# Kernel tuning notes

Hardware: AMD Instinct MI355X
Metric: run time of the kernel (lower is better)

Reference implementation:

```python
import jax, jax.numpy as jnp
import numpy as np

DIM = 1024
NUM_HEADS = 16
HEAD_DIM = DIM // NUM_HEADS
B, S, E = 4, 8192, 2000


def setup_inputs() -> dict:
    key = jax.random.key(0)
    ks = jax.random.split(key, 16)
    sd = 0.02
    inp = {
        "x": jax.random.normal(ks[0], (B, S, DIM), dtype=jnp.float32),
        "src_indices": jax.random.randint(ks[1], (E,), 0, S),
        "dst_indices": jax.random.randint(ks[2], (E,), 0, S),
        # linear weights stored [in, out] (applied as x @ W + b)
        "Wq": jax.random.normal(ks[3], (DIM, DIM), jnp.float32) * sd,
        "bq": jnp.zeros((DIM,), jnp.float32),
        "Wk": jax.random.normal(ks[4], (DIM, DIM), jnp.float32) * sd,
        "bk": jnp.zeros((DIM,), jnp.float32),
        "Wv": jax.random.normal(ks[5], (DIM, DIM), jnp.float32) * sd,
        "bv": jnp.zeros((DIM,), jnp.float32),
        "Wo": jax.random.normal(ks[6], (DIM, DIM), jnp.float32) * sd,
        "bo": jnp.zeros((DIM,), jnp.float32),
        "edge_weight": jax.random.normal(ks[7], (1, NUM_HEADS, 1), jnp.float32),
        "W1": jax.random.normal(ks[8], (2 * HEAD_DIM, HEAD_DIM), jnp.float32) * sd,
        "b1": jnp.zeros((HEAD_DIM,), jnp.float32),
        "W2": jax.random.normal(ks[9], (HEAD_DIM, 1), jnp.float32) * sd,
        "b2": jnp.zeros((1,), jnp.float32),
    }
    return inp


def reference(x, src_indices, dst_indices, Wq, bq, Wk, bk, Wv, bv, Wo, bo,
              edge_weight, W1, b1, W2, b2):
    Bs, Sl, D = x.shape
    H, hd = NUM_HEADS, HEAD_DIM
    scale = hd ** -0.5

    def heads(t):  # [B,S,D] -> [B,H,S,hd]
        return t.reshape(Bs, Sl, H, hd).transpose(0, 2, 1, 3)

    q = heads(x @ Wq + bq)
    k = heads(x @ Wk + bk)
    v = heads(x @ Wv + bv)

    q_src = jnp.take(q, src_indices, axis=2)   # [B,H,E,hd]
    k_dst = jnp.take(k, dst_indices, axis=2)   # [B,H,E,hd]
    v_dst = jnp.take(v, dst_indices, axis=2)   # [B,H,E,hd]

    ef = jnp.concatenate([q_src, k_dst], axis=-1)          # [B,H,E,2hd]
    h = jax.nn.gelu(ef @ W1 + b1, approximate=False)       # [B,H,E,hd]
    scores = (h @ W2 + b2) * scale                         # [B,H,E,1]
    attn = jax.nn.softmax(scores, axis=2)                  # softmax over all edges
    attn = attn * edge_weight[..., None]                   # [1,H,1,1] broadcast

    weighted = attn * v_dst                                # [B,H,E,hd]
    out = jnp.zeros((Bs, H, Sl, hd), x.dtype).at[:, :, src_indices, :].add(weighted)

    final = out.transpose(0, 2, 1, 3).reshape(Bs, Sl, D)
    return final @ Wo + bo
```

## Files before the change

### kernel.cpp

```cpp
#include <hip/hip_runtime.h>
#include <hip/hip_bf16.h>
#include <math.h>

#define DIMK 1024
#define NH 16
#define HD 64
#define BB 4
#define SS 8192
#define EPAD 136

typedef __attribute__((ext_vector_type(8))) short bf16x8;
typedef __attribute__((ext_vector_type(8))) unsigned short ushort8;
typedef __attribute__((ext_vector_type(4))) float f32x4;

#define MFMA16(a, b, c) __builtin_amdgcn_mfma_f32_16x16x32_bf16((a), (b), (c), 0, 0, 0)

__device__ __forceinline__ unsigned short f32_to_bf16_rne(float f) {
  unsigned int u = __float_as_uint(f);
  u = (u + 0x7fffu + ((u >> 16) & 1u)) >> 16;
  return (unsigned short)u;
}
__device__ __forceinline__ float bf16_bits_to_f32(unsigned short b) {
  return __uint_as_float(((unsigned int)b) << 16);
}

__global__ __launch_bounds__(256) void fill_out_kernel(const float4* __restrict__ bo4,
                                                       float4* __restrict__ out, int total4) {
  for (int i = blockIdx.x * 256 + threadIdx.x; i < total4; i += gridDim.x * 256)
    out[i] = bo4[i & 255];
}

__global__ __launch_bounds__(256) void prep_w(const float* __restrict__ W,
                                              unsigned short* __restrict__ WT_hi,
                                              unsigned short* __restrict__ WT_lo) {
  __shared__ float st[64][65];
  const int bk = blockIdx.x * 64, bn = blockIdx.y * 64;
  const int t = threadIdx.x;
  const int lr = t >> 4, lc = (t & 15) * 4;
#pragma unroll
  for (int i = 0; i < 4; i++) {
    int k = lr + i * 16;
    float4 v = *(const float4*)(W + (size_t)(bk + k) * DIMK + bn + lc);
    st[k][lc] = v.x; st[k][lc + 1] = v.y; st[k][lc + 2] = v.z; st[k][lc + 3] = v.w;
  }
  __syncthreads();
#pragma unroll
  for (int i = 0; i < 4; i++) {
    int n = lr + i * 16;
    unsigned long long ph = 0, pl = 0;
#pragma unroll
    for (int j = 0; j < 4; j++) {
      float v = st[lc + j][n];
      unsigned short hb = f32_to_bf16_rne(v);
      unsigned short lb = f32_to_bf16_rne(v - bf16_bits_to_f32(hb));
      ph |= ((unsigned long long)hb) << (16 * j);
      pl |= ((unsigned long long)lb) << (16 * j);
    }
    *(unsigned long long*)(WT_hi + (size_t)(bn + n) * DIMK + bk + lc) = ph;
    *(unsigned long long*)(WT_lo + (size_t)(bn + n) * DIMK + bk + lc) = pl;
  }
}

__global__ __launch_bounds__(256) void prep_w1(const float* __restrict__ W1,
                                               unsigned short* __restrict__ W1Th,
                                               unsigned short* __restrict__ W1Tl) {
  for (int idx = threadIdx.x; idx < 128 * 64; idx += 256) {
    int k = idx >> 6, n = idx & 63;
    float v = W1[idx];
    unsigned short hb = f32_to_bf16_rne(v);
    unsigned short lb = f32_to_bf16_rne(v - bf16_bits_to_f32(hb));
    W1Th[n * 128 + k] = hb;
    W1Tl[n * 128 + k] = lb;
  }
}

__global__ __launch_bounds__(256) void prep_a(const float* __restrict__ X,
                                              const int* __restrict__ gidx,
                                              unsigned short* __restrict__ Ah,
                                              unsigned short* __restrict__ Al, int E) {
  const int row = blockIdx.x;
  const float* sr;
  if (gidx) {
    int b = row / E, e = row - b * E;
    sr = X + ((size_t)b * SS + gidx[e]) * DIMK;
  } else {
    sr = X + (size_t)row * DIMK;
  }
  const int d = threadIdx.x * 4;
  float4 v = *(const float4*)(sr + d);
  float vv[4] = {v.x, v.y, v.z, v.w};
  unsigned long long ph = 0, pl = 0;
#pragma unroll
  for (int i = 0; i < 4; i++) {
    unsigned short hb = f32_to_bf16_rne(vv[i]);
    unsigned short lb = f32_to_bf16_rne(vv[i] - bf16_bits_to_f32(hb));
    ph |= ((unsigned long long)hb) << (16 * i);
    pl |= ((unsigned long long)lb) << (16 * i);
  }
  *(unsigned long long*)(Ah + (size_t)row * DIMK + d) = ph;
  *(unsigned long long*)(Al + (size_t)row * DIMK + d) = pl;
}

__global__ __launch_bounds__(256) void init_table(int* __restrict__ t) {
  t[blockIdx.x * 256 + threadIdx.x] = 0x7fffffff;
}
__global__ __launch_bounds__(256) void build_first(const int* __restrict__ src,
                                                   int* __restrict__ t, int E) {
  int e = blockIdx.x * 256 + threadIdx.x;
  if (e < E) atomicMin(&t[src[e]], e);
}
__global__ __launch_bounds__(256) void read_first(const int* __restrict__ src,
                                                  const int* __restrict__ t,
                                                  int* __restrict__ f, int E) {
  int e = blockIdx.x * 256 + threadIdx.x;
  if (e < E) f[e] = t[src[e]];
}

template <int MODE>
__global__ __launch_bounds__(256) void gemm_bf16p(
    const unsigned short* __restrict__ Ah, const unsigned short* __restrict__ Al,
    const unsigned short* __restrict__ BTh, const unsigned short* __restrict__ BTl,
    const float* __restrict__ bias, const float* __restrict__ bias2,
    float* __restrict__ out, int ldc, int gy,
    const int* __restrict__ fidx, const int* __restrict__ srci, int M, int E) {
  __shared__ unsigned short As_hi[128][40];
  __shared__ unsigned short As_lo[128][40];
  __shared__ unsigned short Bs_hi[128][40];
  __shared__ unsigned short Bs_lo[128][40];

  const int tid = threadIdx.x;
  const int nwg = gridDim.x;
  int w;
  if ((nwg & 7) == 0)
    w = (blockIdx.x & 7) * (nwg >> 3) + (blockIdx.x >> 3);
  else
    w = blockIdx.x;
  const int mt = w / gy, nt = w - mt * gy;
  const int m0 = mt * 128, n0 = nt * 128;

  const int lane = tid & 63, wv = tid >> 6;
  const int wm0 = (wv >> 1) * 64, wn0 = (wv & 1) * 64;

  const int r0 = tid >> 2, q0 = (tid & 3) * 8;
  const int r1 = r0 + 64;
  const size_t a0 = (size_t)((m0 + r0 < M) ? m0 + r0 : M - 1) * DIMK + q0;
  const size_t a1 = (size_t)((m0 + r1 < M) ? m0 + r1 : M - 1) * DIMK + q0;
  const unsigned short* pAh0 = Ah + a0;
  const unsigned short* pAh1 = Ah + a1;
  const unsigned short* pAl0 = Al + a0;
  const unsigned short* pAl1 = Al + a1;
  const size_t b0 = (size_t)(n0 + r0) * DIMK + q0;
  const size_t b1 = (size_t)(n0 + r1) * DIMK + q0;
  const unsigned short* pBh0 = BTh + b0;
  const unsigned short* pBh1 = BTh + b1;
  const unsigned short* pBl0 = BTl + b0;
  const unsigned short* pBl1 = BTl + b1;

  f32x4 acc[4][4];
#pragma unroll
  for (int i = 0; i < 4; i++)
#pragma unroll
    for (int j = 0; j < 4; j++) acc[i][j] = (f32x4){0.f, 0.f, 0.f, 0.f};

  for (int k0 = 0; k0 < DIMK; k0 += 32) {
    ushort8 vAh0 = *(const ushort8*)(pAh0 + k0);
    ushort8 vAh1 = *(const ushort8*)(pAh1 + k0);
    ushort8 vAl0 = *(const ushort8*)(pAl0 + k0);
    ushort8 vAl1 = *(const ushort8*)(pAl1 + k0);
    ushort8 vBh0 = *(const ushort8*)(pBh0 + k0);
    ushort8 vBh1 = *(const ushort8*)(pBh1 + k0);
    ushort8 vBl0 = *(const ushort8*)(pBl0 + k0);
    ushort8 vBl1 = *(const ushort8*)(pBl1 + k0);

    __syncthreads();
    *(ushort8*)&As_hi[r0][q0] = vAh0;
    *(ushort8*)&As_hi[r1][q0] = vAh1;
    *(ushort8*)&As_lo[r0][q0] = vAl0;
    *(ushort8*)&As_lo[r1][q0] = vAl1;
    *(ushort8*)&Bs_hi[r0][q0] = vBh0;
    *(ushort8*)&Bs_hi[r1][q0] = vBh1;
    *(ushort8*)&Bs_lo[r0][q0] = vBl0;
    *(ushort8*)&Bs_lo[r1][q0] = vBl1;
    __syncthreads();

    bf16x8 fah[4], fal[4], fbh[4], fbl[4];
    const int kk = (lane >> 4) * 8;
    const int rr = lane & 15;
#pragma unroll
    for (int f = 0; f < 4; f++) {
      fah[f] = *(bf16x8*)&As_hi[wm0 + f * 16 + rr][kk];
      fal[f] = *(bf16x8*)&As_lo[wm0 + f * 16 + rr][kk];
      fbh[f] = *(bf16x8*)&Bs_hi[wn0 + f * 16 + rr][kk];
      fbl[f] = *(bf16x8*)&Bs_lo[wn0 + f * 16 + rr][kk];
    }
#pragma unroll
    for (int mf = 0; mf < 4; mf++)
#pragma unroll
      for (int nf = 0; nf < 4; nf++) {
        acc[mf][nf] = MFMA16(fah[mf], fbh[nf], acc[mf][nf]);
        acc[mf][nf] = MFMA16(fah[mf], fbl[nf], acc[mf][nf]);
        acc[mf][nf] = MFMA16(fal[mf], fbh[nf], acc[mf][nf]);
      }
  }

  const int cq = lane >> 4, cr = lane & 15;
#pragma unroll
  for (int nf = 0; nf < 4; nf++) {
    const int col = n0 + wn0 + nf * 16 + cr;
    const float bv = (MODE == 0 && bias2 != nullptr && col >= DIMK) ? bias2[col - DIMK]
                                                                    : bias[col & (DIMK - 1)];
#pragma unroll
    for (int mf = 0; mf < 4; mf++) {
#pragma unroll
      for (int r = 0; r < 4; r++) {
        const int mrow = m0 + wm0 + mf * 16 + cq * 4 + r;
        if (mrow >= M) continue;
        if (MODE == 0) {
          out[(size_t)mrow * ldc + col] = acc[mf][nf][r] + bv;
        } else {
          int b = mrow / E, e = mrow - b * E;
          if (fidx[e] == e) {
            int orow = b * SS + srci[e];
            out[(size_t)orow * ldc + col] = acc[mf][nf][r] + bv;
          }
        }
      }
    }
  }
}

__global__ __launch_bounds__(256) void edge_scores_mfma(
    const float* __restrict__ qs, const float* __restrict__ kd, int ldk,
    const unsigned short* __restrict__ W1Th, const unsigned short* __restrict__ W1Tl,
    const float* __restrict__ b1, const float* __restrict__ W2,
    const float* __restrict__ b2, float* __restrict__ scores, int E, int CH) {
  __shared__ unsigned short W1h[64][EPAD], W1l[64][EPAD];
  __shared__ unsigned short EFh[4][16][EPAD], EFl[4][16][EPAD];
  const int tid = threadIdx.x, lane = tid & 63, w = tid >> 6;
  const int bh = blockIdx.x / CH, ch = blockIdx.x - bh * CH;
  const int b = bh >> 4, h = bh & 15;

  for (int idx = tid; idx < 64 * 16; idx += 256) {
    int n = idx >> 4, g = (idx & 15) * 8;
    *(ushort8*)&W1h[n][g] = *(const ushort8*)(W1Th + n * 128 + g);
    *(ushort8*)&W1l[n][g] = *(const ushort8*)(W1Tl + n * 128 + g);
  }
  __syncthreads();

  const int etile = ch * 4 + w;
  const int e0 = etile * 16;
  if (e0 >= E) return;

  const int r = lane >> 2, c0 = (lane & 3) * 16;
  {
    const int er = (e0 + r < E) ? e0 + r : E - 1;
    const float* qrow = qs + ((size_t)(b * E + er)) * DIMK + h * HD + c0;
    const float* krow = kd + ((size_t)(b * E + er)) * (size_t)ldk + h * HD + c0;
    float qv[16], kvv[16];
#pragma unroll
    for (int i = 0; i < 4; i++) {
      *(float4*)&qv[i * 4] = *(const float4*)(qrow + i * 4);
      *(float4*)&kvv[i * 4] = *(const float4*)(krow + i * 4);
    }
    ushort8 qh[2], ql[2], kh[2], kl[2];
#pragma unroll
    for (int g = 0; g < 2; g++)
#pragma unroll
      for (int i = 0; i < 8; i++) {
        float v = qv[g * 8 + i];
        unsigned short hb = f32_to_bf16_rne(v);
        qh[g][i] = hb;
        ql[g][i] = f32_to_bf16_rne(v - bf16_bits_to_f32(hb));
        float v2 = kvv[g * 8 + i];
        unsigned short hb2 = f32_to_bf16_rne(v2);
        kh[g][i] = hb2;
        kl[g][i] = f32_to_bf16_rne(v2 - bf16_bits_to_f32(hb2));
      }
    *(ushort8*)&EFh[w][r][c0] = qh[0];
    *(ushort8*)&EFh[w][r][c0 + 8] = qh[1];
    *(ushort8*)&EFl[w][r][c0] = ql[0];
    *(ushort8*)&EFl[w][r][c0 + 8] = ql[1];
    *(ushort8*)&EFh[w][r][64 + c0] = kh[0];
    *(ushort8*)&EFh[w][r][64 + c0 + 8] = kh[1];
    *(ushort8*)&EFl[w][r][64 + c0] = kl[0];
    *(ushort8*)&EFl[w][r][64 + c0 + 8] = kl[1];
  }
  asm volatile("s_waitcnt lgkmcnt(0)" ::: "memory");
  __builtin_amdgcn_sched_barrier(0);

  f32x4 acc[4];
#pragma unroll
  for (int i = 0; i < 4; i++) acc[i] = (f32x4){0.f, 0.f, 0.f, 0.f};

  const int kk = (lane >> 4) * 8, rr = lane & 15;
#pragma unroll
  for (int ks = 0; ks < 4; ks++) {
    bf16x8 ah = *(bf16x8*)&EFh[w][rr][ks * 32 + kk];
    bf16x8 al = *(bf16x8*)&EFl[w][rr][ks * 32 + kk];
#pragma unroll
    for (int nf = 0; nf < 4; nf++) {
      bf16x8 bh_ = *(bf16x8*)&W1h[nf * 16 + rr][ks * 32 + kk];
      bf16x8 bl_ = *(bf16x8*)&W1l[nf * 16 + rr][ks * 32 + kk];
      acc[nf] = MFMA16(ah, bh_, acc[nf]);
      acc[nf] = MFMA16(ah, bl_, acc[nf]);
      acc[nf] = MFMA16(al, bh_, acc[nf]);
    }
  }

  const int col_l = lane & 15, rq = lane >> 4;
  float w2v[4], b1v[4];
#pragma unroll
  for (int nf = 0; nf < 4; nf++) {
    w2v[nf] = W2[nf * 16 + col_l];
    b1v[nf] = b1[nf * 16 + col_l];
  }
  float p[4];
#pragma unroll
  for (int rr2 = 0; rr2 < 4; rr2++) {
    float s = 0.f;
#pragma unroll
    for (int nf = 0; nf < 4; nf++) {
      float hv = acc[nf][rr2] + b1v[nf];
      hv = 0.5f * hv * (1.f + erff(hv * 0.70710678118654752f));
      s = fmaf(hv, w2v[nf], s);
    }
    p[rr2] = s;
  }
#pragma unroll
  for (int off = 1; off < 16; off <<= 1)
#pragma unroll
    for (int rr2 = 0; rr2 < 4; rr2++) p[rr2] += __shfl_xor(p[rr2], off, 64);

  if (col_l == 0) {
    const float b2v = b2[0];
#pragma unroll
    for (int rr2 = 0; rr2 < 4; rr2++) {
      int e = e0 + rq * 4 + rr2;
      if (e < E) scores[(size_t)(b * NH + h) * E + e] = (p[rr2] + b2v) * 0.125f;
    }
  }
}

__global__ __launch_bounds__(256) void softmax_ew(float* __restrict__ scores,
                                                  const float* __restrict__ ew, int E) {
  const int row = blockIdx.x;
  const int h = row & (NH - 1);
  float* s = scores + (size_t)row * E;
  const int tid = threadIdx.x, lane = tid & 63, w = tid >> 6;
  __shared__ float red[4];

  float vals[8];
  float mx = -1e30f;
#pragma unroll
  for (int i = 0; i < 8; i++) {
    int j = tid + i * 256;
    vals[i] = (j < E) ? s[j] : -1e30f;
    mx = fmaxf(mx, vals[i]);
  }
#pragma unroll
  for (int off = 32; off; off >>= 1) mx = fmaxf(mx, __shfl_xor(mx, off, 64));
  if (lane == 0) red[w] = mx;
  __syncthreads();
  mx = fmaxf(fmaxf(red[0], red[1]), fmaxf(red[2], red[3]));
  __syncthreads();

  float sum = 0.f;
#pragma unroll
  for (int i = 0; i < 8; i++) {
    vals[i] = __expf(vals[i] - mx);
    if (tid + i * 256 < E) sum += vals[i];
  }
#pragma unroll
  for (int off = 32; off; off >>= 1) sum += __shfl_xor(sum, off, 64);
  if (lane == 0) red[w] = sum;
  __syncthreads();
  sum = red[0] + red[1] + red[2] + red[3];

  const float scaleout = ew[h] / sum;
#pragma unroll
  for (int i = 0; i < 8; i++) {
    int j = tid + i * 256;
    if (j < E) s[j] = vals[i] * scaleout;
  }
}

__global__ __launch_bounds__(256) void weight_rows(const float* __restrict__ vd, int ldv,
                                                   const float* __restrict__ attn,
                                                   float* __restrict__ wrow, int E) {
  const int row = blockIdx.x;
  const int b = row / E, e = row - b * E;
  const int d = threadIdx.x * 4;
  const int h = d >> 6;
  const float a = attn[(size_t)(b * NH + h) * E + e];
  float4 v = *(const float4*)(vd + (size_t)row * ldv + d);
  v.x *= a; v.y *= a; v.z *= a; v.w *= a;
  *(float4*)(wrow + (size_t)row * DIMK + d) = v;
}

__global__ __launch_bounds__(256) void dup_add(const int* __restrict__ f,
                                               float* __restrict__ wrow, int E) {
  const int e = blockIdx.x;
  const int fe = f[e];
  if (fe == e) return;
  const int d = threadIdx.x * 4;
#pragma unroll
  for (int b = 0; b < BB; b++) {
    const float4 v = *(const float4*)(wrow + (size_t)(b * E + e) * DIMK + d);
    float* dst = wrow + (size_t)(b * E + fe) * DIMK + d;
    atomicAdd(dst + 0, v.x);
    atomicAdd(dst + 1, v.y);
    atomicAdd(dst + 2, v.z);
    atomicAdd(dst + 3, v.w);
  }
}

extern "C" void kernel_launch(void* const* d_in, const int* in_sizes, int n_in,
                              void* d_out, int out_size, void* d_ws, size_t ws_size,
                              hipStream_t stream) {
  const float* x = (const float*)d_in[0];
  const int* src = (const int*)d_in[1];
  const int* dst = (const int*)d_in[2];
  const float* Wq = (const float*)d_in[3];
  const float* bq = (const float*)d_in[4];
  const float* Wk = (const float*)d_in[5];
  const float* bk = (const float*)d_in[6];
  const float* Wv = (const float*)d_in[7];
  const float* bv = (const float*)d_in[8];
  const float* Wo = (const float*)d_in[9];
  const float* bo = (const float*)d_in[10];
  const float* ew = (const float*)d_in[11];
  const float* W1 = (const float*)d_in[12];
  const float* b1 = (const float*)d_in[13];
  const float* W2 = (const float*)d_in[14];
  const float* b2 = (const float*)d_in[15];
  float* out = (float*)d_out;

  const int E = in_sizes[1];
  const int M = BB * E;

  char* w = (char*)d_ws;
  float* qs = (float*)w; w += (size_t)M * DIMK * 4;
  float* kv = (float*)w; w += (size_t)M * 2048 * 4;
  float* sc = (float*)w; w += (size_t)BB * NH * E * 4;
  int* table = (int*)w; w += (size_t)SS * 4;
  int* fidx = (int*)w; w += (((size_t)E * 4) + 255) & ~(size_t)255;
  const size_t WSZ = (size_t)DIMK * DIMK;
  unsigned short* WqT_hi = (unsigned short*)w;
  unsigned short* WqT_lo = WqT_hi + WSZ;
  unsigned short* WkvT_hi = WqT_lo + WSZ;
  unsigned short* WkvT_lo = WkvT_hi + 2 * WSZ;
  unsigned short* WoT_hi = WkvT_lo + 2 * WSZ;
  unsigned short* WoT_lo = WoT_hi + WSZ;
  unsigned short* Asp_h = WoT_lo + WSZ;
  unsigned short* Asp_l = Asp_h + (size_t)M * DIMK;
  unsigned short* W1Th = Asp_l + (size_t)M * DIMK;
  unsigned short* W1Tl = W1Th + 64 * 128;

  float* wrow = qs;

  const int total4 = BB * SS * (DIMK / 4);
  fill_out_kernel<<<2048, 256, 0, stream>>>((const float4*)bo, (float4*)out, total4);

  dim3 gw(16, 16);
  prep_w<<<gw, 256, 0, stream>>>(Wq, WqT_hi, WqT_lo);
  prep_w<<<gw, 256, 0, stream>>>(Wk, WkvT_hi, WkvT_lo);
  prep_w<<<gw, 256, 0, stream>>>(Wv, WkvT_hi + (size_t)1024 * DIMK, WkvT_lo + (size_t)1024 * DIMK);
  prep_w<<<gw, 256, 0, stream>>>(Wo, WoT_hi, WoT_lo);
  prep_w1<<<1, 256, 0, stream>>>(W1, W1Th, W1Tl);

  init_table<<<SS / 256, 256, 0, stream>>>(table);
  build_first<<<(E + 255) / 256, 256, 0, stream>>>(src, table, E);
  read_first<<<(E + 255) / 256, 256, 0, stream>>>(src, table, fidx, E);

  const int gx = (M + 127) / 128;

  prep_a<<<M, 256, 0, stream>>>(x, src, Asp_h, Asp_l, E);
  gemm_bf16p<0><<<gx * 8, 256, 0, stream>>>(Asp_h, Asp_l, WqT_hi, WqT_lo, bq, nullptr, qs,
                                            DIMK, 8, nullptr, nullptr, M, E);

  prep_a<<<M, 256, 0, stream>>>(x, dst, Asp_h, Asp_l, E);
  gemm_bf16p<0><<<gx * 16, 256, 0, stream>>>(Asp_h, Asp_l, WkvT_hi, WkvT_lo, bk, bv, kv,
                                             2048, 16, nullptr, nullptr, M, E);

  const int etiles = (E + 15) / 16;
  const int CH = (etiles + 3) / 4;
  edge_scores_mfma<<<BB * NH * CH, 256, 0, stream>>>(qs, kv, 2048, W1Th, W1Tl, b1, W2, b2,
                                                     sc, E, CH);

  softmax_ew<<<BB * NH, 256, 0, stream>>>(sc, ew, E);

  weight_rows<<<M, 256, 0, stream>>>(kv + 1024, 2048, sc, wrow, E);
  dup_add<<<E, 256, 0, stream>>>(fidx, wrow, E);
  prep_a<<<M, 256, 0, stream>>>(wrow, nullptr, Asp_h, Asp_l, E);

  gemm_bf16p<1><<<gx * 8, 256, 0, stream>>>(Asp_h, Asp_l, WoT_hi, WoT_lo, bo, nullptr,
                                            out, DIMK, 8, fidx, src, M, E);
}
```

Measured before the change: 417.2 us.

## Rewrite split-bf16 GEMM with swizzled panels, direct-to-LDS loads and 4-stage pipeline

Weights and activations are pre-packed into swizzled K-tile panels, with hi and lo halves laid out as a 96-step K loop (hi·hi, hi·lo, lo·hi). The GEMM now uses 512-thread workgroups with 256-row tiles and global_load_lds async copies into a 4-deep LDS ring, with explicit vmcnt waits. This replaces the per-iteration register staging and two-barrier pattern of the old kernel. The aim is to hide global-load latency and raise MFMA utilisation, at the cost of heavier LDS use, lower occupancy and hand-tuned waitcnt logic.

```diff
diff --git a/kernel.cpp b/kernel.cpp
--- a/kernel.cpp
+++ b/kernel.cpp
@@ -8,9 +8,11 @@
 #define BB 4
 #define SS 8192
 #define EPAD 136
+#define NT 96
 
 typedef __attribute__((ext_vector_type(8))) short bf16x8;
 typedef __attribute__((ext_vector_type(8))) unsigned short ushort8;
+typedef __attribute__((ext_vector_type(4))) unsigned short us4;
 typedef __attribute__((ext_vector_type(4))) float f32x4;
 
 #define MFMA16(a, b, c) __builtin_amdgcn_mfma_f32_16x16x32_bf16((a), (b), (c), 0, 0, 0)
@@ -23,6 +25,10 @@
 __device__ __forceinline__ float bf16_bits_to_f32(unsigned short b) {
   return __uint_as_float(((unsigned int)b) << 16);
 }
+__device__ __forceinline__ void gload16(const void* g, void* l) {
+  __builtin_amdgcn_global_load_lds((const __attribute__((address_space(1))) void*)g,
+                                   (__attribute__((address_space(3))) void*)l, 16, 0, 0);
+}
 
 __global__ __launch_bounds__(256) void fill_out_kernel(const float4* __restrict__ bo4,
                                                        float4* __restrict__ out, int total4) {
@@ -31,8 +37,7 @@
 }
 
 __global__ __launch_bounds__(256) void prep_w(const float* __restrict__ W,
-                                              unsigned short* __restrict__ WT_hi,
-                                              unsigned short* __restrict__ WT_lo) {
+                                              unsigned short* __restrict__ Bpan, int pnoff) {
   __shared__ float st[64][65];
   const int bk = blockIdx.x * 64, bn = blockIdx.y * 64;
   const int t = threadIdx.x;
@@ -44,20 +49,25 @@
     st[k][lc] = v.x; st[k][lc + 1] = v.y; st[k][lc + 2] = v.z; st[k][lc + 3] = v.w;
   }
   __syncthreads();
+  const int ktile = (bk + lc) >> 5, c = lc & 31;
 #pragma unroll
   for (int i = 0; i < 4; i++) {
-    int n = lr + i * 16;
-    unsigned long long ph = 0, pl = 0;
+    const int nl = lr + i * 16;
+    const int n = bn + nl;
+    const int r = n & 127, pn = (n >> 7) + pnoff;
+    const int q = (c >> 3) ^ ((r >> 1) & 3);
+    const size_t byteoff = (size_t)r * 64 + q * 16 + (c & 7) * 2;
+    us4 hv, lv;
 #pragma unroll
     for (int j = 0; j < 4; j++) {
-      float v = st[lc + j][n];
+      float v = st[lc + j][nl];
       unsigned short hb = f32_to_bf16_rne(v);
-      unsigned short lb = f32_to_bf16_rne(v - bf16_bits_to_f32(hb));
-      ph |= ((unsigned long long)hb) << (16 * j);
-      pl |= ((unsigned long long)lb) << (16 * j);
-    }
-    *(unsigned long long*)(WT_hi + (size_t)(bn + n) * DIMK + bk + lc) = ph;
-    *(unsigned long long*)(WT_lo + (size_t)(bn + n) * DIMK + bk + lc) = pl;
+      hv[j] = hb;
+      lv[j] = f32_to_bf16_rne(v - bf16_bits_to_f32(hb));
+    }
+    char* base = (char*)Bpan;
+    *(us4*)(base + (((size_t)pn * 64 + ktile) << 13) + byteoff) = hv;
+    *(us4*)(base + (((size_t)pn * 64 + 32 + ktile) << 13) + byteoff) = lv;
   }
 }
 
@@ -68,37 +78,41 @@
     int k = idx >> 6, n = idx & 63;
     float v = W1[idx];
     unsigned short hb = f32_to_bf16_rne(v);
-    unsigned short lb = f32_to_bf16_rne(v - bf16_bits_to_f32(hb));
     W1Th[n * 128 + k] = hb;
-    W1Tl[n * 128 + k] = lb;
+    W1Tl[n * 128 + k] = f32_to_bf16_rne(v - bf16_bits_to_f32(hb));
   }
 }
 
 __global__ __launch_bounds__(256) void prep_a(const float* __restrict__ X,
                                               const int* __restrict__ gidx,
-                                              unsigned short* __restrict__ Ah,
-                                              unsigned short* __restrict__ Al, int E) {
+                                              unsigned short* __restrict__ Apan, int M, int E) {
   const int row = blockIdx.x;
-  const float* sr;
-  if (gidx) {
-    int b = row / E, e = row - b * E;
-    sr = X + ((size_t)b * SS + gidx[e]) * DIMK;
-  } else {
-    sr = X + (size_t)row * DIMK;
-  }
-  const int d = threadIdx.x * 4;
-  float4 v = *(const float4*)(sr + d);
-  float vv[4] = {v.x, v.y, v.z, v.w};
-  unsigned long long ph = 0, pl = 0;
-#pragma unroll
-  for (int i = 0; i < 4; i++) {
-    unsigned short hb = f32_to_bf16_rne(vv[i]);
-    unsigned short lb = f32_to_bf16_rne(vv[i] - bf16_bits_to_f32(hb));
-    ph |= ((unsigned long long)hb) << (16 * i);
-    pl |= ((unsigned long long)lb) << (16 * i);
-  }
-  *(unsigned long long*)(Ah + (size_t)row * DIMK + d) = ph;
-  *(unsigned long long*)(Al + (size_t)row * DIMK + d) = pl;
+  const int r = row & 255, mt = row >> 8;
+  const int c0 = threadIdx.x * 4;
+  const int kt = c0 >> 5, c = c0 & 31;
+  const int q = (c >> 3) ^ ((r >> 1) & 3);
+  const size_t byteoff = (size_t)r * 64 + q * 16 + (c & 7) * 2;
+  char* base = (char*)Apan;
+  us4 hv = (us4){0, 0, 0, 0}, lv = (us4){0, 0, 0, 0};
+  if (row < M) {
+    const float* sr;
+    if (gidx) {
+      int b = row / E, e = row - b * E;
+      sr = X + ((size_t)b * SS + gidx[e]) * DIMK;
+    } else {
+      sr = X + (size_t)row * DIMK;
+    }
+    float4 v = *(const float4*)(sr + c0);
+    float vv[4] = {v.x, v.y, v.z, v.w};
+#pragma unroll
+    for (int i = 0; i < 4; i++) {
+      unsigned short hb = f32_to_bf16_rne(vv[i]);
+      hv[i] = hb;
+      lv[i] = f32_to_bf16_rne(vv[i] - bf16_bits_to_f32(hb));
+    }
+  }
+  *(us4*)(base + (((size_t)(mt * 64 + kt)) << 14) + byteoff) = hv;
+  *(us4*)(base + (((size_t)(mt * 64 + 32 + kt)) << 14) + byteoff) = lv;
 }
 
 __global__ __launch_bounds__(256) void init_table(int* __restrict__ t) {
@@ -116,104 +130,120 @@
   if (e < E) f[e] = t[src[e]];
 }
 
-template <int MODE>
-__global__ __launch_bounds__(256) void gemm_bf16p(
-    const unsigned short* __restrict__ Ah, const unsigned short* __restrict__ Al,
-    const unsigned short* __restrict__ BTh, const unsigned short* __restrict__ BTl,
+template <int BN, int MODE>
+__global__ __launch_bounds__(512, 2) void gemm8(
+    const unsigned short* __restrict__ Apan, const unsigned short* __restrict__ Bpan,
     const float* __restrict__ bias, const float* __restrict__ bias2,
-    float* __restrict__ out, int ldc, int gy,
+    float* __restrict__ out, int ldc, int nty,
     const int* __restrict__ fidx, const int* __restrict__ srci, int M, int E) {
-  __shared__ unsigned short As_hi[128][40];
-  __shared__ unsigned short As_lo[128][40];
-  __shared__ unsigned short Bs_hi[128][40];
-  __shared__ unsigned short Bs_lo[128][40];
-
-  const int tid = threadIdx.x;
-  const int nwg = gridDim.x;
-  int w;
-  if ((nwg & 7) == 0)
-    w = (blockIdx.x & 7) * (nwg >> 3) + (blockIdx.x >> 3);
-  else
-    w = blockIdx.x;
-  const int mt = w / gy, nt = w - mt * gy;
-  const int m0 = mt * 128, n0 = nt * 128;
-
-  const int lane = tid & 63, wv = tid >> 6;
-  const int wm0 = (wv >> 1) * 64, wn0 = (wv & 1) * 64;
-
-  const int r0 = tid >> 2, q0 = (tid & 3) * 8;
-  const int r1 = r0 + 64;
-  const size_t a0 = (size_t)((m0 + r0 < M) ? m0 + r0 : M - 1) * DIMK + q0;
-  const size_t a1 = (size_t)((m0 + r1 < M) ? m0 + r1 : M - 1) * DIMK + q0;
-  const unsigned short* pAh0 = Ah + a0;
-  const unsigned short* pAh1 = Ah + a1;
-  const unsigned short* pAl0 = Al + a0;
-  const unsigned short* pAl1 = Al + a1;
-  const size_t b0 = (size_t)(n0 + r0) * DIMK + q0;
-  const size_t b1 = (size_t)(n0 + r1) * DIMK + q0;
-  const unsigned short* pBh0 = BTh + b0;
-  const unsigned short* pBh1 = BTh + b1;
-  const unsigned short* pBl0 = BTl + b0;
-  const unsigned short* pBl1 = BTl + b1;
-
-  f32x4 acc[4][4];
-#pragma unroll
-  for (int i = 0; i < 4; i++)
-#pragma unroll
-    for (int j = 0; j < 4; j++) acc[i][j] = (f32x4){0.f, 0.f, 0.f, 0.f};
-
-  for (int k0 = 0; k0 < DIMK; k0 += 32) {
-    ushort8 vAh0 = *(const ushort8*)(pAh0 + k0);
-    ushort8 vAh1 = *(const ushort8*)(pAh1 + k0);
-    ushort8 vAl0 = *(const ushort8*)(pAl0 + k0);
-    ushort8 vAl1 = *(const ushort8*)(pAl1 + k0);
-    ushort8 vBh0 = *(const ushort8*)(pBh0 + k0);
-    ushort8 vBh1 = *(const ushort8*)(pBh1 + k0);
-    ushort8 vBl0 = *(const ushort8*)(pBl0 + k0);
-    ushort8 vBl1 = *(const ushort8*)(pBl1 + k0);
-
-    __syncthreads();
-    *(ushort8*)&As_hi[r0][q0] = vAh0;
-    *(ushort8*)&As_hi[r1][q0] = vAh1;
-    *(ushort8*)&As_lo[r0][q0] = vAl0;
-    *(ushort8*)&As_lo[r1][q0] = vAl1;
-    *(ushort8*)&Bs_hi[r0][q0] = vBh0;
-    *(ushort8*)&Bs_hi[r1][q0] = vBh1;
-    *(ushort8*)&Bs_lo[r0][q0] = vBl0;
-    *(ushort8*)&Bs_lo[r1][q0] = vBl1;
-    __syncthreads();
-
-    bf16x8 fah[4], fal[4], fbh[4], fbl[4];
-    const int kk = (lane >> 4) * 8;
-    const int rr = lane & 15;
-#pragma unroll
-    for (int f = 0; f < 4; f++) {
-      fah[f] = *(bf16x8*)&As_hi[wm0 + f * 16 + rr][kk];
-      fal[f] = *(bf16x8*)&As_lo[wm0 + f * 16 + rr][kk];
-      fbh[f] = *(bf16x8*)&Bs_hi[wn0 + f * 16 + rr][kk];
-      fbl[f] = *(bf16x8*)&Bs_lo[wn0 + f * 16 + rr][kk];
-    }
-#pragma unroll
-    for (int mf = 0; mf < 4; mf++)
-#pragma unroll
-      for (int nf = 0; nf < 4; nf++) {
-        acc[mf][nf] = MFMA16(fah[mf], fbh[nf], acc[mf][nf]);
-        acc[mf][nf] = MFMA16(fah[mf], fbl[nf], acc[mf][nf]);
-        acc[mf][nf] = MFMA16(fal[mf], fbh[nf], acc[mf][nf]);
+  constexpr int NF = BN / 64;
+  constexpr int BTILE = BN * 32;
+  __shared__ unsigned short ldsA[4][8192];
+  __shared__ unsigned short ldsB[4][BTILE];
+
+  const int tid = threadIdx.x, lane = tid & 63, wv = tid >> 6;
+  const int wr = wv >> 2, wc = wv & 3;
+
+  const int w = (blockIdx.x & 7) * ((int)gridDim.x >> 3) + ((int)blockIdx.x >> 3);
+  const int mt = w / nty, nt_ = w - mt * nty;
+  const int m0 = mt * 256, n0 = nt_ * BN;
+
+  const int rr = lane & 15, lq = lane >> 4;
+  const int swz = (rr >> 1) & 3;
+  const int aoff = (wr * 128 + rr) * 32 + ((lq ^ swz) << 3);
+  const int boff = (wc * (BN / 4) + rr) * 32 + ((lq ^ swz) << 3);
+
+  const char* Apb = (const char*)Apan + ((size_t)(mt * 64) << 14);
+  const char* Bpb = (const char*)Bpan;
+  const int stoff = wv * 1024 + lane * 16;
+
+  f32x4 acc[8][NF];
+#pragma unroll
+  for (int i = 0; i < 8; i++)
+#pragma unroll
+    for (int j = 0; j < NF; j++) acc[i][j] = (f32x4){0.f, 0.f, 0.f, 0.f};
+
+  auto stageA = [&](int kt, int buf) {
+    const int apk = kt < 64 ? kt : kt - 64;
+    const char* s = Apb + ((size_t)apk << 14) + stoff;
+    gload16(s, &ldsA[buf][wv * 512]);
+    gload16(s + 8192, &ldsA[buf][wv * 512 + 4096]);
+  };
+  auto stageB = [&](int kt, int buf) {
+    const int bpk = kt < 32 ? kt : kt - 32;
+    if (BN == 256) {
+      const char* s0 = Bpb + (((size_t)(2 * nt_) * 64 + bpk) << 13) + stoff;
+      const char* s1 = Bpb + (((size_t)(2 * nt_ + 1) * 64 + bpk) << 13) + stoff;
+      gload16(s0, &ldsB[buf][wv * 512]);
+      gload16(s1, &ldsB[buf][wv * 512 + 4096]);
+    } else {
+      const char* s0 = Bpb + (((size_t)nt_ * 64 + bpk) << 13) + stoff;
+      gload16(s0, &ldsB[buf][wv * 512]);
+    }
+  };
+
+  stageA(0, 0); stageB(0, 0);
+  stageA(1, 1); stageB(1, 1);
+  stageA(2, 2); stageB(2, 2);
+  if constexpr (BN == 256) asm volatile("s_waitcnt vmcnt(8)" ::: "memory");
+  else asm volatile("s_waitcnt vmcnt(6)" ::: "memory");
+  __builtin_amdgcn_sched_barrier(0);
+  __builtin_amdgcn_s_barrier();
+
+  for (int kt = 0; kt < NT; ++kt) {
+    const int buf = kt & 3;
+    const unsigned short* Al = ldsA[buf];
+    const unsigned short* Bl = ldsB[buf];
+    const int sb = (kt + 3) & 3;
+    const bool st = (kt + 3 < NT);
+
+    bf16x8 fb[NF];
+#pragma unroll
+    for (int nf = 0; nf < NF; ++nf) fb[nf] = *(const bf16x8*)(Bl + boff + nf * 512);
+    bf16x8 fa[4];
+#pragma unroll
+    for (int mf = 0; mf < 4; ++mf) fa[mf] = *(const bf16x8*)(Al + aoff + mf * 512);
+    if (st) stageA(kt + 3, sb);
+#pragma unroll
+    for (int mf = 0; mf < 4; ++mf)
+#pragma unroll
+      for (int nf = 0; nf < NF; ++nf) acc[mf][nf] = MFMA16(fa[mf], fb[nf], acc[mf][nf]);
+
+    bf16x8 fa2[4];
+#pragma unroll
+    for (int mf = 0; mf < 4; ++mf) fa2[mf] = *(const bf16x8*)(Al + aoff + (mf + 4) * 512);
+    if (st) stageB(kt + 3, sb);
+#pragma unroll
+    for (int mf = 0; mf < 4; ++mf)
+#pragma unroll
+      for (int nf = 0; nf < NF; ++nf) acc[mf + 4][nf] = MFMA16(fa2[mf], fb[nf], acc[mf + 4][nf]);
+
+    if (kt < NT - 1) {
+      if (kt + 3 < NT) {
+        if constexpr (BN == 256) asm volatile("s_waitcnt vmcnt(8)" ::: "memory");
+        else asm volatile("s_waitcnt vmcnt(6)" ::: "memory");
+      } else if (kt + 2 < NT) {
+        if constexpr (BN == 256) asm volatile("s_waitcnt vmcnt(4)" ::: "memory");
+        else asm volatile("s_waitcnt vmcnt(3)" ::: "memory");
+      } else {
+        asm volatile("s_waitcnt vmcnt(0)" ::: "memory");
       }
+      __builtin_amdgcn_sched_barrier(0);
+      __builtin_amdgcn_s_barrier();
+    }
   }
 
   const int cq = lane >> 4, cr = lane & 15;
 #pragma unroll
-  for (int nf = 0; nf < 4; nf++) {
-    const int col = n0 + wn0 + nf * 16 + cr;
+  for (int nf = 0; nf < NF; ++nf) {
+    const int col = n0 + wc * (BN / 4) + nf * 16 + cr;
     const float bv = (MODE == 0 && bias2 != nullptr && col >= DIMK) ? bias2[col - DIMK]
                                                                     : bias[col & (DIMK - 1)];
 #pragma unroll
-    for (int mf = 0; mf < 4; mf++) {
-#pragma unroll
-      for (int r = 0; r < 4; r++) {
-        const int mrow = m0 + wm0 + mf * 16 + cq * 4 + r;
+    for (int mf = 0; mf < 8; ++mf) {
+#pragma unroll
+      for (int r = 0; r < 4; ++r) {
+        const int mrow = m0 + wr * 128 + mf * 16 + cq * 4 + r;
         if (mrow >= M) continue;
         if (MODE == 0) {
           out[(size_t)mrow * ldc + col] = acc[mf][nf][r] + bv;
@@ -292,15 +322,15 @@
 #pragma unroll
   for (int i = 0; i < 4; i++) acc[i] = (f32x4){0.f, 0.f, 0.f, 0.f};
 
-  const int kk = (lane >> 4) * 8, rr = lane & 15;
+  const int kk = (lane >> 4) * 8, rrl = lane & 15;
 #pragma unroll
   for (int ks = 0; ks < 4; ks++) {
-    bf16x8 ah = *(bf16x8*)&EFh[w][rr][ks * 32 + kk];
-    bf16x8 al = *(bf16x8*)&EFl[w][rr][ks * 32 + kk];
+    bf16x8 ah = *(bf16x8*)&EFh[w][rrl][ks * 32 + kk];
+    bf16x8 al = *(bf16x8*)&EFl[w][rrl][ks * 32 + kk];
 #pragma unroll
     for (int nf = 0; nf < 4; nf++) {
-      bf16x8 bh_ = *(bf16x8*)&W1h[nf * 16 + rr][ks * 32 + kk];
-      bf16x8 bl_ = *(bf16x8*)&W1l[nf * 16 + rr][ks * 32 + kk];
+      bf16x8 bh_ = *(bf16x8*)&W1h[nf * 16 + rrl][ks * 32 + kk];
+      bf16x8 bl_ = *(bf16x8*)&W1l[nf * 16 + rrl][ks * 32 + kk];
       acc[nf] = MFMA16(ah, bh_, acc[nf]);
       acc[nf] = MFMA16(ah, bl_, acc[nf]);
       acc[nf] = MFMA16(al, bh_, acc[nf]);
@@ -437,6 +467,8 @@
 
   const int E = in_sizes[1];
   const int M = BB * E;
+  const int gx = (M + 255) / 256;
+  const int Mpad = gx * 256;
 
   char* w = (char*)d_ws;
   float* qs = (float*)w; w += (size_t)M * DIMK * 4;
@@ -444,17 +476,12 @@
   float* sc = (float*)w; w += (size_t)BB * NH * E * 4;
   int* table = (int*)w; w += (size_t)SS * 4;
   int* fidx = (int*)w; w += (((size_t)E * 4) + 255) & ~(size_t)255;
-  const size_t WSZ = (size_t)DIMK * DIMK;
-  unsigned short* WqT_hi = (unsigned short*)w;
-  unsigned short* WqT_lo = WqT_hi + WSZ;
-  unsigned short* WkvT_hi = WqT_lo + WSZ;
-  unsigned short* WkvT_lo = WkvT_hi + 2 * WSZ;
-  unsigned short* WoT_hi = WkvT_lo + 2 * WSZ;
-  unsigned short* WoT_lo = WoT_hi + WSZ;
-  unsigned short* Asp_h = WoT_lo + WSZ;
-  unsigned short* Asp_l = Asp_h + (size_t)M * DIMK;
-  unsigned short* W1Th = Asp_l + (size_t)M * DIMK;
-  unsigned short* W1Tl = W1Th + 64 * 128;
+  unsigned short* W1Th = (unsigned short*)w; w += 64 * 128 * 2;
+  unsigned short* W1Tl = (unsigned short*)w; w += 64 * 128 * 2;
+  unsigned short* Bq = (unsigned short*)w; w += (size_t)8 * 64 * 8192;
+  unsigned short* Bkv = (unsigned short*)w; w += (size_t)16 * 64 * 8192;
+  unsigned short* Bo = (unsigned short*)w; w += (size_t)8 * 64 * 8192;
+  unsigned short* Apan = (unsigned short*)w; w += (size_t)gx * 64 * 16384;
 
   float* wrow = qs;
 
@@ -462,25 +489,23 @@
   fill_out_kernel<<<2048, 256, 0, stream>>>((const float4*)bo, (float4*)out, total4);
 
   dim3 gw(16, 16);
-  prep_w<<<gw, 256, 0, stream>>>(Wq, WqT_hi, WqT_lo);
-  prep_w<<<gw, 256, 0, stream>>>(Wk, WkvT_hi, WkvT_lo);
-  prep_w<<<gw, 256, 0, stream>>>(Wv, WkvT_hi + (size_t)1024 * DIMK, WkvT_lo + (size_t)1024 * DIMK);
-  prep_w<<<gw, 256, 0, stream>>>(Wo, WoT_hi, WoT_lo);
+  prep_w<<<gw, 256, 0, stream>>>(Wq, Bq, 0);
+  prep_w<<<gw, 256, 0, stream>>>(Wk, Bkv, 0);
+  prep_w<<<gw, 256, 0, stream>>>(Wv, Bkv, 8);
+  prep_w<<<gw, 256, 0, stream>>>(Wo, Bo, 0);
   prep_w1<<<1, 256, 0, stream>>>(W1, W1Th, W1Tl);
 
   init_table<<<SS / 256, 256, 0, stream>>>(table);
   build_first<<<(E + 255) / 256, 256, 0, stream>>>(src, table, E);
   read_first<<<(E + 255) / 256, 256, 0, stream>>>(src, table, fidx, E);
 
-  const int gx = (M + 127) / 128;
-
-  prep_a<<<M, 256, 0, stream>>>(x, src, Asp_h, Asp_l, E);
-  gemm_bf16p<0><<<gx * 8, 256, 0, stream>>>(Asp_h, Asp_l, WqT_hi, WqT_lo, bq, nullptr, qs,
-                                            DIMK, 8, nullptr, nullptr, M, E);
-
-  prep_a<<<M, 256, 0, stream>>>(x, dst, Asp_h, Asp_l, E);
-  gemm_bf16p<0><<<gx * 16, 256, 0, stream>>>(Asp_h, Asp_l, WkvT_hi, WkvT_lo, bk, bv, kv,
-                                             2048, 16, nullptr, nullptr, M, E);
+  prep_a<<<Mpad, 256, 0, stream>>>(x, src, Apan, M, E);
+  gemm8<128, 0><<<gx * 8, 512, 0, stream>>>(Apan, Bq, bq, nullptr, qs, DIMK, 8,
+                                            nullptr, nullptr, M, E);
+
+  prep_a<<<Mpad, 256, 0, stream>>>(x, dst, Apan, M, E);
+  gemm8<256, 0><<<gx * 8, 512, 0, stream>>>(Apan, Bkv, bk, bv, kv, 2048, 8,
+                                            nullptr, nullptr, M, E);
 
   const int etiles = (E + 15) / 16;
   const int CH = (etiles + 3) / 4;
@@ -491,8 +516,8 @@
 
   weight_rows<<<M, 256, 0, stream>>>(kv + 1024, 2048, sc, wrow, E);
   dup_add<<<E, 256, 0, stream>>>(fidx, wrow, E);
-  prep_a<<<M, 256, 0, stream>>>(wrow, nullptr, Asp_h, Asp_l, E);
-
-  gemm_bf16p<1><<<gx * 8, 256, 0, stream>>>(Asp_h, Asp_l, WoT_hi, WoT_lo, bo, nullptr,
-                                            out, DIMK, 8, fidx, src, M, E);
-}
+  prep_a<<<Mpad, 256, 0, stream>>>(wrow, nullptr, Apan, M, E);
+
+  gemm8<128, 1><<<gx * 8, 512, 0, stream>>>(Apan, Bo, bo, nullptr, out, DIMK, 8,
+                                            fidx, src, M, E);
+}
```

After: 432.8 us. 1.04x slower.
